# Optimization experiments

Hardware: AMD Instinct MI355X
Metric: run time of the kernel (lower is better)

Reference implementation:

```python
import jax, jax.numpy as jnp
import numpy as np

BLOCK_SIZE = 128  # config.block_size; first query block skips intra-block causal mask (faithful to source)
NEG = -1e9       # the module uses -1e9, not -inf, for masking and m_i init


def setup_inputs() -> dict:
    key = jax.random.key(0)
    kq, kk, kv, km = jax.random.split(key, 4)
    B, S, H, D = 2, 2048, 16, 64
    q = jax.random.normal(kq, (B, S, H, D), dtype=jnp.float32)
    k = jax.random.normal(kk, (B, S, H, D), dtype=jnp.float32)
    v = jax.random.normal(kv, (B, S, H, D), dtype=jnp.float32)
    mask = jax.random.randint(km, (B, S), 0, 2).astype(bool)
    mask = mask.at[:, 0].set(True)  # keep first key attendable
    return {"q": q, "k": k, "v": v, "mask": mask}


def reference(q, k, v, mask):
    # q,k,v: [B,S,H,D]; mask: [B,S] bool (True = attend)
    B, S, H, D = q.shape
    scale = 1.0 / np.sqrt(D)
    # config.normalize_query=True -> F.normalize(q, dim=-1) (eps=1e-12)
    qn = q / jnp.maximum(jnp.linalg.norm(q, axis=-1, keepdims=True), 1e-12)
    # scores: [B,S(query),H,S(key)]
    scores = jnp.einsum('bshd,bkhd->bshk', qn, k) * scale
    qi = jnp.arange(S)[:, None]
    ki = jnp.arange(S)[None, :]
    # Faithful causal structure of the blocked PyTorch fallback:
    #  - keys limited to k <= q (triu(diagonal=block_start+1) masking)
    #  - EXCEPT the first query block (block_start==0), where the intra-block
    #    causal mask is skipped (keys still limited to the first block).
    allowed = (ki <= qi) | ((qi < BLOCK_SIZE) & (ki < BLOCK_SIZE))  # [S,S]
    scores = jnp.where(allowed[None, :, None, :], scores, NEG)
    scores = jnp.where(mask[:, None, None, :], scores, NEG)
    p = jax.nn.softmax(scores, axis=-1)
    out = jnp.einsum('bshk,bkhd->bshd', p, v)
    return out
```

## Files before the change

### kernel.cpp

```cpp
#include <hip/hip_runtime.h>
#include <stdint.h>

typedef __attribute__((ext_vector_type(8))) short short8;
typedef __attribute__((ext_vector_type(4))) float floatx4;
typedef __attribute__((ext_vector_type(4))) unsigned int uintx4;
typedef __attribute__((ext_vector_type(2))) unsigned int uintx2;

#define S_LEN 2048
#define NHEAD 16
#define DHEAD 64
#define KB    64
#define NTILE 32
#define PL_BYTES (S_LEN * DHEAD * 2)
#define VOFF  (2 * NHEAD * PL_BYTES)
#define MOFF  (2 * VOFF)
#define WS_NEEDED ((size_t)MOFF + 2 * 4096)
#define NEGINF (-__builtin_inff())
#define LOG2E 1.4426950408889634f

#define GLOAD_LDS16(gp, lp) \
    __builtin_amdgcn_global_load_lds((const __attribute__((address_space(1))) unsigned int*)(gp), \
                                     (__attribute__((address_space(3))) unsigned int*)(lp), 16, 0, 0)

static __device__ __forceinline__ unsigned f2bf(float f) {
    union { float f; unsigned u; } w; w.f = f;
    return (w.u + 0x7FFFu + ((w.u >> 16) & 1u)) >> 16;
}

static __device__ __forceinline__ unsigned cvtpk(float lo, float hi) {
    unsigned r;
    asm("v_cvt_pk_bf16_f32 %0, %1, %2" : "=v"(r) : "v"(lo), "v"(hi));
    return r;
}

static __device__ __forceinline__ floatx4 mfma16(short8 a, short8 b, floatx4 c) {
    return __builtin_amdgcn_mfma_f32_16x16x32_bf16(a, b, c, 0, 0, 0);
}

__global__ __launch_bounds__(256) void prep_kernel(
    const float* __restrict__ kg, const float* __restrict__ vg,
    const int* __restrict__ mg, char* __restrict__ ws)
{
    __shared__ unsigned short Tl[64 * 72];
    const int bid = blockIdx.x;
    const int t   = bid & 31;
    const int bh  = bid >> 5;
    const int b   = bh >> 4, h = bh & 15;
    const int tid = threadIdx.x;
    char* kpre = ws + (size_t)bh * PL_BYTES;
    char* vpre = ws + VOFF + (size_t)bh * PL_BYTES;

    {
        const int r  = tid >> 2;
        const int c0 = (tid & 3) * 32;
        const int X  = (r & 7) << 4;
        const size_t grow = (((size_t)b * S_LEN + t * 64 + r) * NHEAD + h) * DHEAD;
        #pragma unroll
        for (int cc = 0; cc < 2; ++cc) {
            const int c  = c0 + 16 * cc;
            const int d0 = (c ^ X) >> 1;
            floatx4 f0 = *(const floatx4*)(kg + grow + d0);
            floatx4 f1 = *(const floatx4*)(kg + grow + d0 + 4);
            uintx4 pk = (uintx4){ f2bf(f0[0]) | (f2bf(f0[1]) << 16),
                                  f2bf(f0[2]) | (f2bf(f0[3]) << 16),
                                  f2bf(f1[0]) | (f2bf(f1[1]) << 16),
                                  f2bf(f1[2]) | (f2bf(f1[3]) << 16) };
            *(uintx4*)(kpre + t * 8192 + r * 128 + c) = pk;
        }
    }
    {
        const int key = tid >> 2;
        const int d0  = (tid & 3) * 16;
        const float vz = mg[(size_t)b * S_LEN + t * 64 + key] ? 1.f : 0.f;
        const size_t grow = (((size_t)b * S_LEN + t * 64 + key) * NHEAD + h) * DHEAD;
        #pragma unroll
        for (int q = 0; q < 4; ++q) {
            floatx4 f = *(const floatx4*)(vg + grow + d0 + 4 * q);
            #pragma unroll
            for (int ii = 0; ii < 4; ++ii)
                Tl[(d0 + 4 * q + ii) * 72 + key] = (unsigned short)f2bf(f[ii] * vz);
        }
    }
    __syncthreads();
    {
        const int d  = tid >> 2;
        const int c0 = (tid & 3) * 32;
        const int Xv = (d & 7) << 4;
        #pragma unroll
        for (int cc = 0; cc < 2; ++cc) {
            const int c   = c0 + 16 * cc;
            const int pp0 = (c ^ Xv) >> 1;
            const int blk = pp0 >> 5;
            const int a   = (pp0 & 31) >> 3;
            unsigned short vals[8];
            #pragma unroll
            for (int i = 0; i < 8; ++i) {
                const int key = 32 * blk + ((i < 4) ? (4 * a + i) : (16 + 4 * a + i - 4));
                vals[i] = Tl[d * 72 + key];
            }
            *(uintx4*)(vpre + t * 8192 + d * 128 + c) = *(const uintx4*)vals;
        }
    }
    if (h == 0 && tid < 64) {
        const int key = tid;
        const int gg = (key >> 2) & 3, lo = key & 3;
        const int ks = key >> 5,      hi = (key >> 4) & 1;
        const unsigned short mv = mg[(size_t)b * S_LEN + t * 64 + key] ? 0x3F80 : 0;
        *(unsigned short*)(ws + MOFF + (size_t)b * 4096 + t * 128
                           + gg * 32 + ks * 16 + (4 * hi + lo) * 2) = mv;
    }
}

__global__ __launch_bounds__(512, 4) void fa3_main(
    const float* __restrict__ qg, const char* __restrict__ ws,
    float* __restrict__ og)
{
    __shared__ char smem[49152];
    unsigned short* Qs = (unsigned short*)smem;
    char* KsB = smem + 16384;
    char* VsB = smem + 32768;

    const int tid  = threadIdx.x;
    const int bid  = blockIdx.x;
    const int b    = bid >> 8;
    const int bh   = (b << 4) | (bid & 15);
    const int rpair= (bid >> 4) & 15;
    const int qb   = b ? rpair : 15 - rpair;
    const int h    = bh & 15;
    const int w    = tid >> 6;
    const int lane = tid & 63;
    const int g    = lane >> 4;
    const int lm   = lane & 15;
    const int kh   = w >> 2;
    const int wq   = w & 3;
    const char* kpre = ws + (size_t)bh * PL_BYTES;
    const char* vpre = ws + VOFF + (size_t)bh * PL_BYTES;
    const char* mgf  = ws + MOFF + (size_t)b * 4096;
    const int nkt = (qb == 0) ? 2 : (2 * qb + 2);

    GLOAD_LDS16(kpre + tid * 16, KsB + tid * 16);
    GLOAD_LDS16(vpre + tid * 16, VsB + tid * 16);

    {
        const int r  = tid >> 2;
        const int q0 = tid & 3;
        const float* src = qg + (((size_t)b * S_LEN + (size_t)qb * 128 + r) * NHEAD + h) * DHEAD + q0 * 16;
        floatx4 f0 = *(const floatx4*)(src + 0);
        floatx4 f1 = *(const floatx4*)(src + 4);
        floatx4 f2 = *(const floatx4*)(src + 8);
        floatx4 f3 = *(const floatx4*)(src + 12);
        float ssq = 0.f;
        #pragma unroll
        for (int i = 0; i < 4; ++i)
            ssq += f0[i]*f0[i] + f1[i]*f1[i] + f2[i]*f2[i] + f3[i]*f3[i];
        ssq += __shfl_xor(ssq, 1);
        ssq += __shfl_xor(ssq, 2);
        const float sc = (0.125f * LOG2E) / fmaxf(sqrtf(ssq), 1e-12f);
        float fv[16];
        #pragma unroll
        for (int i = 0; i < 4; ++i) { fv[i]=f0[i]; fv[4+i]=f1[i]; fv[8+i]=f2[i]; fv[12+i]=f3[i]; }
        unsigned pk[8];
        #pragma unroll
        for (int i = 0; i < 8; ++i)
            pk[i] = cvtpk(fv[2*i]*sc, fv[2*i+1]*sc);
        const int X = (r & 7) << 4;
        char* qp = (char*)Qs + r * 128;
        *(uintx4*)(qp + ((32*q0)      ^ X)) = (uintx4){pk[0],pk[1],pk[2],pk[3]};
        *(uintx4*)(qp + ((32*q0 + 16) ^ X)) = (uintx4){pk[4],pk[5],pk[6],pk[7]};
    }
    asm volatile("s_waitcnt vmcnt(0)" ::: "memory");
    __syncthreads();

    const int Xl = (lm & 7) << 4;
    short8 qf[2][2];
    #pragma unroll
    for (int grp = 0; grp < 2; ++grp) {
        const int row = wq * 32 + grp * 16 + lm;
        const char* base = (const char*)Qs + row * 128;
        #pragma unroll
        for (int ksd = 0; ksd < 2; ++ksd)
            qf[grp][ksd] = *(const short8*)(base + ((64*ksd + 16*g) ^ Xl));
    }

    floatx4 oacc[2][4];
    floatx4 dacc[2];
    #pragma unroll
    for (int grp = 0; grp < 2; ++grp) {
        dacc[grp] = (floatx4){0.f,0.f,0.f,0.f};
        #pragma unroll
        for (int nt = 0; nt < 4; ++nt) oacc[grp][nt] = (floatx4){0.f,0.f,0.f,0.f};
    }
    const int qgl0 = qb * 128 + wq * 32 + lm;

    int cur = 0;
    for (int kt = 0; kt < nkt; ++kt) {
        if (kt + 1 < nkt) {
            const size_t tb = (size_t)(kt + 1) * 8192;
            GLOAD_LDS16(kpre + tb + tid * 16, KsB + (cur ^ 1) * 8192 + tid * 16);
            GLOAD_LDS16(vpre + tb + tid * 16, VsB + (cur ^ 1) * 8192 + tid * 16);
        }
        const short8 mf = *(const short8*)(mgf + kt * 128 + g * 32 + kh * 16);

        floatx4 st[2][2];
        #pragma unroll
        for (int grp = 0; grp < 2; ++grp)
            #pragma unroll
            for (int mt = 0; mt < 2; ++mt) st[grp][mt] = (floatx4){-8.f,-8.f,-8.f,-8.f};
        const char* kbase = KsB + cur * 8192 + kh * 4096 + lm * 128;
        __builtin_amdgcn_s_setprio(1);
        #pragma unroll
        for (int ksd = 0; ksd < 2; ++ksd) {
            #pragma unroll
            for (int mt = 0; mt < 2; ++mt) {
                short8 kf = *(const short8*)(kbase + mt * 2048 + ((64*ksd + 16*g) ^ Xl));
                st[0][mt] = mfma16(kf, qf[0][ksd], st[0][mt]);
                st[1][mt] = mfma16(kf, qf[1][ksd], st[1][mt]);
            }
        }
        __builtin_amdgcn_s_setprio(0);

        if ((qb >= 1) && (kt >= 2 * qb)) {
            #pragma unroll
            for (int mt = 0; mt < 2; ++mt)
                #pragma unroll
                for (int j = 0; j < 4; ++j) {
                    const int kgl = kt * KB + kh * 32 + mt * 16 + 4 * g + j;
                    if (kgl > qgl0)      st[0][mt][j] = -10000.f;
                    if (kgl > qgl0 + 16) st[1][mt][j] = -10000.f;
                }
        }

        short8 pa[2];
        #pragma unroll
        for (int grp = 0; grp < 2; ++grp) {
            float p[8];
            #pragma unroll
            for (int mt = 0; mt < 2; ++mt)
                #pragma unroll
                for (int j = 0; j < 4; ++j)
                    p[mt * 4 + j] = exp2f(st[grp][mt][j]);
            union { short8 s; uintx4 u; } pu;
            pu.u = (uintx4){ cvtpk(p[0], p[1]), cvtpk(p[2], p[3]),
                             cvtpk(p[4], p[5]), cvtpk(p[6], p[7]) };
            pa[grp] = pu.s;
        }
        __builtin_amdgcn_s_setprio(1);
        dacc[0] = mfma16(pa[0], mf, dacc[0]);
        dacc[1] = mfma16(pa[1], mf, dacc[1]);
        {
            const char* vbase = VsB + cur * 8192 + lm * 128;
            #pragma unroll
            for (int nt = 0; nt < 4; ++nt) {
                short8 vf = *(const short8*)(vbase + nt * 2048 + ((64*kh + 16*g) ^ Xl));
                oacc[0][nt] = mfma16(pa[0], vf, oacc[0][nt]);
                oacc[1][nt] = mfma16(pa[1], vf, oacc[1][nt]);
            }
        }
        __builtin_amdgcn_s_setprio(0);

        asm volatile("s_waitcnt vmcnt(0)" ::: "memory");
        __syncthreads();
        cur ^= 1;
    }

    floatx4* rbuf = (floatx4*)(smem + 16384);
    float*   dbuf = (float*)smem;
    if (kh == 1) {
        const int tpos = (w - 4) * 64 + lane;
        #pragma unroll
        for (int grp = 0; grp < 2; ++grp) {
            #pragma unroll
            for (int nt = 0; nt < 4; ++nt)
                rbuf[(grp * 4 + nt) * 256 + tpos] = oacc[grp][nt];
            if (lm == 0) {
                #pragma unroll
                for (int j = 0; j < 4; ++j)
                    dbuf[wq * 32 + grp * 16 + 4 * g + j] = dacc[grp][j];
            }
        }
    }
    __syncthreads();
    if (kh == 0) {
        const int tpos = w * 64 + lane;
        #pragma unroll
        for (int grp = 0; grp < 2; ++grp) {
            #pragma unroll
            for (int nt = 0; nt < 4; ++nt)
                oacc[grp][nt] += rbuf[(grp * 4 + nt) * 256 + tpos];
            #pragma unroll
            for (int j = 0; j < 4; ++j) {
                const float den = dacc[grp][j] + dbuf[wq * 32 + grp * 16 + 4 * g + j];
                const float invj = 1.0f / den;
                const int row = qb * 128 + wq * 32 + grp * 16 + 4 * g + j;
                float* dst = og + (((size_t)b * S_LEN + row) * NHEAD + h) * DHEAD + lm;
                #pragma unroll
                for (int nt = 0; nt < 4; ++nt) dst[nt * 16] = oacc[grp][nt][j] * invj;
            }
        }
    }
}

__global__ __launch_bounds__(512) void fa3_fallback(
    const float* __restrict__ qg, const float* __restrict__ kg,
    const float* __restrict__ vg, const int* __restrict__ mg,
    float* __restrict__ og)
{
    __shared__ unsigned short Qs[128 * DHEAD];
    __shared__ unsigned short Ks2[KB * DHEAD];
    __shared__ unsigned short Vt[DHEAD * KB];
    __shared__ float Ms[KB];

    const int tid  = threadIdx.x;
    const int bid  = blockIdx.x;
    const int qb   = 15 - (bid >> 5);
    const int bh   = bid & 31;
    const int b    = bh >> 4;
    const int h    = bh & 15;
    const int w    = tid >> 6;
    const int lane = tid & 63;
    const int g    = lane >> 4;
    const int lm   = lane & 15;

    {
        const int r  = tid >> 2;
        const int q0 = tid & 3;
        const float* src = qg + (((size_t)b * S_LEN + (size_t)qb * 128 + r) * NHEAD + h) * DHEAD + q0 * 16;
        floatx4 f0 = *(const floatx4*)(src + 0);
        floatx4 f1 = *(const floatx4*)(src + 4);
        floatx4 f2 = *(const floatx4*)(src + 8);
        floatx4 f3 = *(const floatx4*)(src + 12);
        float ssq = 0.f;
        #pragma unroll
        for (int i = 0; i < 4; ++i)
            ssq += f0[i]*f0[i] + f1[i]*f1[i] + f2[i]*f2[i] + f3[i]*f3[i];
        ssq += __shfl_xor(ssq, 1);
        ssq += __shfl_xor(ssq, 2);
        const float sc = 0.125f / fmaxf(sqrtf(ssq), 1e-12f);
        float fv[16];
        #pragma unroll
        for (int i = 0; i < 4; ++i) { fv[i]=f0[i]; fv[4+i]=f1[i]; fv[8+i]=f2[i]; fv[12+i]=f3[i]; }
        unsigned pk[8];
        #pragma unroll
        for (int i = 0; i < 8; ++i)
            pk[i] = f2bf(fv[2*i]*sc) | (f2bf(fv[2*i+1]*sc) << 16);
        const int X = (r & 7) << 4;
        char* qp = (char*)Qs + r * 128;
        *(uintx4*)(qp + ((32*q0)      ^ X)) = (uintx4){pk[0],pk[1],pk[2],pk[3]};
        *(uintx4*)(qp + ((32*q0 + 16) ^ X)) = (uintx4){pk[4],pk[5],pk[6],pk[7]};
    }
    __syncthreads();

    short8 qf[2];
    {
        const int row = w * 16 + lm;
        const int X = (row & 7) << 4;
        const char* base = (const char*)Qs + row * 128;
        #pragma unroll
        for (int ks = 0; ks < 2; ++ks) {
            union { short8 s; uintx2 u[2]; } u;
            u.u[0] = *(const uintx2*)(base + ((64*ks + 8*g)      ^ X));
            u.u[1] = *(const uintx2*)(base + ((64*ks + 8*g + 32) ^ X));
            qf[ks] = u.s;
        }
    }

    floatx4 oacc[4];
    #pragma unroll
    for (int nt = 0; nt < 4; ++nt) oacc[nt] = (floatx4){0.f,0.f,0.f,0.f};
    float mrun = NEGINF, lrun = 0.f;
    const int q_glob = qb * 128 + w * 16 + lm;
    const int nkt = (qb == 0) ? 2 : (2 * qb + 2);

    for (int kt = 0; kt < nkt; ++kt) {
        const int kb0 = kt * KB;
        {
            const int r = tid >> 3;
            const int o = tid & 7;
            const size_t goff = (((size_t)b * S_LEN + kb0 + r) * NHEAD + h) * DHEAD + o * 8;
            floatx4 a0 = *(const floatx4*)(kg + goff);
            floatx4 a1 = *(const floatx4*)(kg + goff + 4);
            floatx4 c0 = *(const floatx4*)(vg + goff);
            floatx4 c1 = *(const floatx4*)(vg + goff + 4);
            uintx4 kw = (uintx4){ f2bf(a0[0]) | (f2bf(a0[1])<<16),
                                  f2bf(a0[2]) | (f2bf(a0[3])<<16),
                                  f2bf(a1[0]) | (f2bf(a1[1])<<16),
                                  f2bf(a1[2]) | (f2bf(a1[3])<<16) };
            *(uintx4*)((char*)Ks2 + r*128 + ((16*o) ^ ((r & 7) << 4))) = kw;
            float cv[8];
            #pragma unroll
            for (int i = 0; i < 4; ++i) { cv[i] = c0[i]; cv[4+i] = c1[i]; }
            #pragma unroll
            for (int i = 0; i < 8; ++i) {
                const int d = 8*o + i;
                Vt[d*64 + (r ^ (((i ^ o) & 7) << 3))] = (unsigned short)f2bf(cv[i]);
            }
            if (tid < KB) Ms[tid] = mg[(size_t)b * S_LEN + kb0 + tid] ? 0.f : NEGINF;
        }
        __syncthreads();

        floatx4 st[4];
        #pragma unroll
        for (int mt = 0; mt < 4; ++mt) st[mt] = (floatx4){0.f,0.f,0.f,0.f};
        #pragma unroll
        for (int ks = 0; ks < 2; ++ks) {
            #pragma unroll
            for (int mt = 0; mt < 4; ++mt) {
                const int row = mt * 16 + lm;
                const int X = (row & 7) << 4;
                const char* base = (const char*)Ks2 + row * 128;
                union { short8 s; uintx2 u[2]; } u;
                u.u[0] = *(const uintx2*)(base + ((64*ks + 8*g)      ^ X));
                u.u[1] = *(const uintx2*)(base + ((64*ks + 8*g + 32) ^ X));
                st[mt] = mfma16(u.s, qf[ks], st[mt]);
            }
        }

        const bool diag = (qb > 0) && (kt >= 2 * qb);
        float sv[16];
        #pragma unroll
        for (int mt = 0; mt < 4; ++mt) {
            #pragma unroll
            for (int j = 0; j < 4; ++j) {
                const int kl = mt * 16 + 4 * g + j;
                float s = st[mt][j] + Ms[kl];
                if (diag && (kb0 + kl > q_glob)) s = NEGINF;
                sv[mt * 4 + j] = s;
            }
        }

        float rmax = sv[0];
        #pragma unroll
        for (int i = 1; i < 16; ++i) rmax = fmaxf(rmax, sv[i]);
        rmax = fmaxf(rmax, __shfl_xor(rmax, 16));
        rmax = fmaxf(rmax, __shfl_xor(rmax, 32));
        const float mnew = fmaxf(mrun, rmax);
        const float cf = __expf(mrun - mnew);
        float p[16], psum = 0.f;
        #pragma unroll
        for (int i = 0; i < 16; ++i) { p[i] = __expf(sv[i] - mnew); psum += p[i]; }
        psum += __shfl_xor(psum, 16);
        psum += __shfl_xor(psum, 32);
        lrun = lrun * cf + psum;
        mrun = mnew;

        float cj[4];
        #pragma unroll
        for (int j = 0; j < 4; ++j) cj[j] = __shfl(cf, 20 * g + j);
        #pragma unroll
        for (int nt = 0; nt < 4; ++nt)
            #pragma unroll
            for (int j = 0; j < 4; ++j) oacc[nt][j] *= cj[j];

        short8 pa[2];
        #pragma unroll
        for (int ks = 0; ks < 2; ++ks)
            #pragma unroll
            for (int i = 0; i < 8; ++i)
                pa[ks][i] = (short)f2bf(p[(2*ks + (i>>2))*4 + (i&3)]);

        #pragma unroll
        for (int nt = 0; nt < 4; ++nt) {
            const int d = 16 * nt + lm;
            const int xz = (((d & 7) ^ ((d >> 3) & 7)) & 7) << 4;
            const char* vb = (const char*)Vt + d * 128;
            #pragma unroll
            for (int ks = 0; ks < 2; ++ks) {
                union { short8 s; uintx2 u[2]; } vu;
                vu.u[0] = *(const uintx2*)(vb + ((64*ks + 8*g)      ^ xz));
                vu.u[1] = *(const uintx2*)(vb + ((64*ks + 8*g + 32) ^ xz));
                oacc[nt] = mfma16(pa[ks], vu.s, oacc[nt]);
            }
        }
        __syncthreads();
    }

    const float inv = 1.0f / lrun;
    #pragma unroll
    for (int j = 0; j < 4; ++j) {
        const float invj = __shfl(inv, 20 * g + j);
        const int row = qb * 128 + w * 16 + 4 * g + j;
        float* dst = og + (((size_t)b * S_LEN + row) * NHEAD + h) * DHEAD + lm;
        #pragma unroll
        for (int nt = 0; nt < 4; ++nt) dst[nt * 16] = oacc[nt][j] * invj;
    }
}

extern "C" void kernel_launch(void* const* d_in, const int* in_sizes, int n_in,
                              void* d_out, int out_size, void* d_ws, size_t ws_size,
                              hipStream_t stream)
{
    const float* q = (const float*)d_in[0];
    const float* k = (const float*)d_in[1];
    const float* v = (const float*)d_in[2];
    const int*   m = (const int*)d_in[3];
    float* out = (float*)d_out;
    (void)in_sizes; (void)n_in; (void)out_size;
    if (ws_size >= WS_NEEDED) {
        prep_kernel<<<dim3(1024), dim3(256), 0, stream>>>(k, v, m, (char*)d_ws);
        fa3_main<<<dim3(512), dim3(512), 0, stream>>>(q, (const char*)d_ws, out);
    } else {
        fa3_fallback<<<dim3(512), dim3(512), 0, stream>>>(q, k, v, m, out);
    }
}
```

Measured before the change: 50.46 us.

## Split KV range across two blocks with 256-row query tiles and combine kernel

The query tile per block grows from 128 to 256 rows, so each wave now holds four 16-row groups and every K/V fragment is reused across more MFMAs. The key range for each query tile is split into two halves handled by separate blocks. Each block writes unnormalized partial outputs and denominators to workspace, and a new combine kernel sums the two halves and normalizes. This balances causal work across blocks and raises data reuse, at the cost of an extra kernel launch, about 32MB of partial-result traffic, and higher register and LDS use (64KB LDS).

```diff
diff --git a/kernel.cpp b/kernel.cpp
--- a/kernel.cpp
+++ b/kernel.cpp
@@ -14,7 +14,11 @@
 #define PL_BYTES (S_LEN * DHEAD * 2)
 #define VOFF  (2 * NHEAD * PL_BYTES)
 #define MOFF  (2 * VOFF)
-#define WS_NEEDED ((size_t)MOFF + 2 * 4096)
+#define PO0   (MOFF + 8192)
+#define PO1   (PO0 + 256 * 65536)
+#define DN0   (PO1 + 256 * 65536)
+#define DN1   (DN0 + 262144)
+#define WS_NEEDED ((size_t)DN1 + 262144)
 #define NEGINF (-__builtin_inff())
 #define LOG2E 1.4426950408889634f
 
@@ -112,20 +116,20 @@
 }
 
 __global__ __launch_bounds__(512, 4) void fa3_main(
-    const float* __restrict__ qg, const char* __restrict__ ws,
-    float* __restrict__ og)
+    const float* __restrict__ qg, char* __restrict__ ws)
 {
-    __shared__ char smem[49152];
+    __shared__ char smem[65536];
     unsigned short* Qs = (unsigned short*)smem;
-    char* KsB = smem + 16384;
-    char* VsB = smem + 32768;
+    char* KsB = smem + 32768;
+    char* VsB = smem + 49152;
 
     const int tid  = threadIdx.x;
     const int bid  = blockIdx.x;
-    const int b    = bid >> 8;
-    const int bh   = (b << 4) | (bid & 15);
-    const int rpair= (bid >> 4) & 15;
-    const int qb   = b ? rpair : 15 - rpair;
+    const int half = bid >> 8;
+    const int r256 = bid & 255;
+    const int qb   = half ? (7 - (r256 >> 5)) : (r256 >> 5);
+    const int bh   = r256 & 31;
+    const int b    = bh >> 4;
     const int h    = bh & 15;
     const int w    = tid >> 6;
     const int lane = tid & 63;
@@ -136,15 +140,18 @@
     const char* kpre = ws + (size_t)bh * PL_BYTES;
     const char* vpre = ws + VOFF + (size_t)bh * PL_BYTES;
     const char* mgf  = ws + MOFF + (size_t)b * 4096;
-    const int nkt = (qb == 0) ? 2 : (2 * qb + 2);
-
-    GLOAD_LDS16(kpre + tid * 16, KsB + tid * 16);
-    GLOAD_LDS16(vpre + tid * 16, VsB + tid * 16);
-
-    {
-        const int r  = tid >> 2;
+    const int H   = 2 * qb + 2;
+    const int kt0 = half * H, kt1 = kt0 + H;
+    const int slot = qb * 32 + bh;
+
+    GLOAD_LDS16(kpre + (size_t)kt0 * 8192 + tid * 16, KsB + tid * 16);
+    GLOAD_LDS16(vpre + (size_t)kt0 * 8192 + tid * 16, VsB + tid * 16);
+
+    #pragma unroll
+    for (int rr = 0; rr < 2; ++rr) {
+        const int r  = rr * 128 + (tid >> 2);
         const int q0 = tid & 3;
-        const float* src = qg + (((size_t)b * S_LEN + (size_t)qb * 128 + r) * NHEAD + h) * DHEAD + q0 * 16;
+        const float* src = qg + (((size_t)b * S_LEN + (size_t)qb * 256 + r) * NHEAD + h) * DHEAD + q0 * 16;
         floatx4 f0 = *(const floatx4*)(src + 0);
         floatx4 f1 = *(const floatx4*)(src + 4);
         floatx4 f2 = *(const floatx4*)(src + 8);
@@ -172,38 +179,38 @@
     __syncthreads();
 
     const int Xl = (lm & 7) << 4;
-    short8 qf[2][2];
+    short8 qf[4][2];
     #pragma unroll
-    for (int grp = 0; grp < 2; ++grp) {
-        const int row = wq * 32 + grp * 16 + lm;
+    for (int grp = 0; grp < 4; ++grp) {
+        const int row = wq * 64 + grp * 16 + lm;
         const char* base = (const char*)Qs + row * 128;
         #pragma unroll
         for (int ksd = 0; ksd < 2; ++ksd)
             qf[grp][ksd] = *(const short8*)(base + ((64*ksd + 16*g) ^ Xl));
     }
 
-    floatx4 oacc[2][4];
-    floatx4 dacc[2];
+    floatx4 oacc[4][4];
+    floatx4 dacc[4];
     #pragma unroll
-    for (int grp = 0; grp < 2; ++grp) {
+    for (int grp = 0; grp < 4; ++grp) {
         dacc[grp] = (floatx4){0.f,0.f,0.f,0.f};
         #pragma unroll
         for (int nt = 0; nt < 4; ++nt) oacc[grp][nt] = (floatx4){0.f,0.f,0.f,0.f};
     }
-    const int qgl0 = qb * 128 + wq * 32 + lm;
+    const int qwmin = qb * 256 + wq * 64;
 
     int cur = 0;
-    for (int kt = 0; kt < nkt; ++kt) {
-        if (kt + 1 < nkt) {
+    for (int kt = kt0; kt < kt1; ++kt) {
+        if (kt + 1 < kt1) {
             const size_t tb = (size_t)(kt + 1) * 8192;
             GLOAD_LDS16(kpre + tb + tid * 16, KsB + (cur ^ 1) * 8192 + tid * 16);
             GLOAD_LDS16(vpre + tb + tid * 16, VsB + (cur ^ 1) * 8192 + tid * 16);
         }
         const short8 mf = *(const short8*)(mgf + kt * 128 + g * 32 + kh * 16);
 
-        floatx4 st[2][2];
-        #pragma unroll
-        for (int grp = 0; grp < 2; ++grp)
+        floatx4 st[4][2];
+        #pragma unroll
+        for (int grp = 0; grp < 4; ++grp)
             #pragma unroll
             for (int mt = 0; mt < 2; ++mt) st[grp][mt] = (floatx4){-8.f,-8.f,-8.f,-8.f};
         const char* kbase = KsB + cur * 8192 + kh * 4096 + lm * 128;
@@ -213,26 +220,38 @@
             #pragma unroll
             for (int mt = 0; mt < 2; ++mt) {
                 short8 kf = *(const short8*)(kbase + mt * 2048 + ((64*ksd + 16*g) ^ Xl));
-                st[0][mt] = mfma16(kf, qf[0][ksd], st[0][mt]);
-                st[1][mt] = mfma16(kf, qf[1][ksd], st[1][mt]);
+                #pragma unroll
+                for (int grp = 0; grp < 4; ++grp)
+                    st[grp][mt] = mfma16(kf, qf[grp][ksd], st[grp][mt]);
             }
         }
         __builtin_amdgcn_s_setprio(0);
 
-        if ((qb >= 1) && (kt >= 2 * qb)) {
-            #pragma unroll
-            for (int mt = 0; mt < 2; ++mt)
+        short8 vf[4];
+        {
+            const char* vbase = VsB + cur * 8192 + lm * 128;
+            #pragma unroll
+            for (int nt = 0; nt < 4; ++nt)
+                vf[nt] = *(const short8*)(vbase + nt * 2048 + ((64*kh + 16*g) ^ Xl));
+        }
+
+        if ((kt * 64 + 63 > qwmin) && (qb > 0 || kt >= 2)) {
+            #pragma unroll
+            for (int grp = 0; grp < 4; ++grp) {
+                const int qgl = qwmin + grp * 16 + lm;
                 #pragma unroll
-                for (int j = 0; j < 4; ++j) {
-                    const int kgl = kt * KB + kh * 32 + mt * 16 + 4 * g + j;
-                    if (kgl > qgl0)      st[0][mt][j] = -10000.f;
-                    if (kgl > qgl0 + 16) st[1][mt][j] = -10000.f;
-                }
-        }
-
-        short8 pa[2];
-        #pragma unroll
-        for (int grp = 0; grp < 2; ++grp) {
+                for (int mt = 0; mt < 2; ++mt)
+                    #pragma unroll
+                    for (int j = 0; j < 4; ++j) {
+                        const int kgl = kt * 64 + kh * 32 + mt * 16 + 4 * g + j;
+                        if (kgl > qgl) st[grp][mt][j] = -10000.f;
+                    }
+            }
+        }
+
+        short8 pa[4];
+        #pragma unroll
+        for (int grp = 0; grp < 4; ++grp) {
             float p[8];
             #pragma unroll
             for (int mt = 0; mt < 2; ++mt)
@@ -245,16 +264,12 @@
             pa[grp] = pu.s;
         }
         __builtin_amdgcn_s_setprio(1);
-        dacc[0] = mfma16(pa[0], mf, dacc[0]);
-        dacc[1] = mfma16(pa[1], mf, dacc[1]);
-        {
-            const char* vbase = VsB + cur * 8192 + lm * 128;
-            #pragma unroll
-            for (int nt = 0; nt < 4; ++nt) {
-                short8 vf = *(const short8*)(vbase + nt * 2048 + ((64*kh + 16*g) ^ Xl));
-                oacc[0][nt] = mfma16(pa[0], vf, oacc[0][nt]);
-                oacc[1][nt] = mfma16(pa[1], vf, oacc[1][nt]);
-            }
+        #pragma unroll
+        for (int grp = 0; grp < 4; ++grp) {
+            dacc[grp] = mfma16(pa[grp], mf, dacc[grp]);
+            #pragma unroll
+            for (int nt = 0; nt < 4; ++nt)
+                oacc[grp][nt] = mfma16(pa[grp], vf[nt], oacc[grp][nt]);
         }
         __builtin_amdgcn_s_setprio(0);
 
@@ -263,41 +278,73 @@
         cur ^= 1;
     }
 
-    floatx4* rbuf = (floatx4*)(smem + 16384);
-    float*   dbuf = (float*)smem;
+    floatx4* rbuf = (floatx4*)smem;
     if (kh == 1) {
-        const int tpos = (w - 4) * 64 + lane;
-        #pragma unroll
-        for (int grp = 0; grp < 2; ++grp) {
+        #pragma unroll
+        for (int grp = 0; grp < 4; ++grp)
             #pragma unroll
             for (int nt = 0; nt < 4; ++nt)
-                rbuf[(grp * 4 + nt) * 256 + tpos] = oacc[grp][nt];
-            if (lm == 0) {
-                #pragma unroll
-                for (int j = 0; j < 4; ++j)
-                    dbuf[wq * 32 + grp * 16 + 4 * g + j] = dacc[grp][j];
-            }
-        }
+                rbuf[wq * 1024 + (grp * 4 + nt) * 64 + lane] = oacc[grp][nt];
     }
     __syncthreads();
     if (kh == 0) {
-        const int tpos = w * 64 + lane;
-        #pragma unroll
-        for (int grp = 0; grp < 2; ++grp) {
+        #pragma unroll
+        for (int grp = 0; grp < 4; ++grp)
             #pragma unroll
             for (int nt = 0; nt < 4; ++nt)
-                oacc[grp][nt] += rbuf[(grp * 4 + nt) * 256 + tpos];
+                oacc[grp][nt] += rbuf[wq * 1024 + (grp * 4 + nt) * 64 + lane];
+    }
+    __syncthreads();
+    float* dbuf = (float*)smem;
+    if (kh == 1 && lm == 0) {
+        #pragma unroll
+        for (int grp = 0; grp < 4; ++grp)
+            #pragma unroll
+            for (int j = 0; j < 4; ++j)
+                dbuf[wq * 64 + grp * 16 + 4 * g + j] = dacc[grp][j];
+    }
+    __syncthreads();
+    if (kh == 0) {
+        float* po = (float*)(ws + (half ? PO1 : PO0) + (size_t)slot * 65536);
+        float* pd = (float*)(ws + (half ? DN1 : DN0) + (size_t)slot * 1024);
+        #pragma unroll
+        for (int grp = 0; grp < 4; ++grp)
             #pragma unroll
             for (int j = 0; j < 4; ++j) {
-                const float den = dacc[grp][j] + dbuf[wq * 32 + grp * 16 + 4 * g + j];
-                const float invj = 1.0f / den;
-                const int row = qb * 128 + wq * 32 + grp * 16 + 4 * g + j;
-                float* dst = og + (((size_t)b * S_LEN + row) * NHEAD + h) * DHEAD + lm;
+                const int row = wq * 64 + grp * 16 + 4 * g + j;
                 #pragma unroll
-                for (int nt = 0; nt < 4; ++nt) dst[nt * 16] = oacc[grp][nt][j] * invj;
-            }
-        }
-    }
+                for (int nt = 0; nt < 4; ++nt)
+                    po[row * 64 + nt * 16 + lm] = oacc[grp][nt][j];
+                if (lm == 0)
+                    pd[row] = dacc[grp][j] + dbuf[row];
+            }
+    }
+}
+
+__global__ __launch_bounds__(256) void fa3_combine(
+    const char* __restrict__ ws, float* __restrict__ og)
+{
+    const int i0  = (blockIdx.x * 256 + threadIdx.x) * 8;
+    const int d   = i0 & 63;
+    int rem       = i0 >> 6;
+    const int h   = rem & 15;  rem >>= 4;
+    const int row = rem & 2047;
+    const int b   = rem >> 11;
+    const int qb  = row >> 8;
+    const int q   = row & 255;
+    const int slot = qb * 32 + b * 16 + h;
+    const float* p0 = (const float*)(ws + PO0 + (size_t)slot * 65536) + q * 64 + d;
+    const float* p1 = (const float*)(ws + PO1 + (size_t)slot * 65536) + q * 64 + d;
+    const float den = ((const float*)(ws + DN0 + (size_t)slot * 1024))[q]
+                    + ((const float*)(ws + DN1 + (size_t)slot * 1024))[q];
+    const float inv = 1.0f / den;
+    floatx4 a0 = *(const floatx4*)p0, a1 = *(const floatx4*)(p0 + 4);
+    floatx4 b0 = *(const floatx4*)p1, b1 = *(const floatx4*)(p1 + 4);
+    floatx4 o0, o1;
+    #pragma unroll
+    for (int i = 0; i < 4; ++i) { o0[i] = (a0[i] + b0[i]) * inv; o1[i] = (a1[i] + b1[i]) * inv; }
+    *(floatx4*)(og + i0)     = o0;
+    *(floatx4*)(og + i0 + 4) = o1;
 }
 
 __global__ __launch_bounds__(512) void fa3_fallback(
@@ -497,7 +544,8 @@
     (void)in_sizes; (void)n_in; (void)out_size;
     if (ws_size >= WS_NEEDED) {
         prep_kernel<<<dim3(1024), dim3(256), 0, stream>>>(k, v, m, (char*)d_ws);
-        fa3_main<<<dim3(512), dim3(512), 0, stream>>>(q, (const char*)d_ws, out);
+        fa3_main<<<dim3(512), dim3(512), 0, stream>>>(q, (char*)d_ws);
+        fa3_combine<<<dim3(2048), dim3(256), 0, stream>>>((const char*)d_ws, out);
     } else {
         fa3_fallback<<<dim3(512), dim3(512), 0, stream>>>(q, k, v, m, out);
     }
```

New measurement: 164.5 us. 226% more time.

## Triple-buffer K/V tiles with prefetch distance two and partial vmcnt waits

Applied to the files above, without the earlier changes.

Moves the K/V LDS staging from double to triple buffering. Tiles are prefetched two iterations ahead, and each iteration waits with a partial vmcnt before a single barrier instead of draining all loads and syncing at the end of the loop. The mask fragment is also loaded one tile ahead, and the first QK MFMA takes a constant -8 accumulator directly. The epilogue reduction gets a different rbuf indexing and extra barriers. This cuts load-latency stalls per iteration, at the cost of LDS rising from 48KB to 64KB, which may lower occupancy below the 4 blocks the launch bounds request.

```diff
diff --git a/kernel.cpp b/kernel.cpp
--- a/kernel.cpp
+++ b/kernel.cpp
@@ -115,10 +115,10 @@
     const float* __restrict__ qg, const char* __restrict__ ws,
     float* __restrict__ og)
 {
-    __shared__ char smem[49152];
+    __shared__ char smem[65536];
     unsigned short* Qs = (unsigned short*)smem;
     char* KsB = smem + 16384;
-    char* VsB = smem + 32768;
+    char* VsB = smem + 40960;
 
     const int tid  = threadIdx.x;
     const int bid  = blockIdx.x;
@@ -168,7 +168,6 @@
         *(uintx4*)(qp + ((32*q0)      ^ X)) = (uintx4){pk[0],pk[1],pk[2],pk[3]};
         *(uintx4*)(qp + ((32*q0 + 16) ^ X)) = (uintx4){pk[4],pk[5],pk[6],pk[7]};
     }
-    asm volatile("s_waitcnt vmcnt(0)" ::: "memory");
     __syncthreads();
 
     const int Xl = (lm & 7) << 4;
@@ -182,6 +181,12 @@
             qf[grp][ksd] = *(const short8*)(base + ((64*ksd + 16*g) ^ Xl));
     }
 
+    short8 mfn = *(const short8*)(mgf + 0 * 128 + g * 32 + kh * 16);
+    if (nkt > 1) {
+        GLOAD_LDS16(kpre + 8192 + tid * 16, KsB + 8192 + tid * 16);
+        GLOAD_LDS16(vpre + 8192 + tid * 16, VsB + 8192 + tid * 16);
+    }
+
     floatx4 oacc[2][4];
     floatx4 dacc[2];
     #pragma unroll
@@ -190,32 +195,41 @@
         #pragma unroll
         for (int nt = 0; nt < 4; ++nt) oacc[grp][nt] = (floatx4){0.f,0.f,0.f,0.f};
     }
+    floatx4 NEG8 = (floatx4){-8.f,-8.f,-8.f,-8.f};
+    asm volatile("" : "+v"(NEG8));
     const int qgl0 = qb * 128 + wq * 32 + lm;
 
     int cur = 0;
     for (int kt = 0; kt < nkt; ++kt) {
-        if (kt + 1 < nkt) {
-            const size_t tb = (size_t)(kt + 1) * 8192;
-            GLOAD_LDS16(kpre + tb + tid * 16, KsB + (cur ^ 1) * 8192 + tid * 16);
-            GLOAD_LDS16(vpre + tb + tid * 16, VsB + (cur ^ 1) * 8192 + tid * 16);
-        }
-        const short8 mf = *(const short8*)(mgf + kt * 128 + g * 32 + kh * 16);
+        if (kt + 1 < nkt) { asm volatile("s_waitcnt vmcnt(2)" ::: "memory"); }
+        else              { asm volatile("s_waitcnt vmcnt(0)" ::: "memory"); }
+        __builtin_amdgcn_s_barrier();
+        __builtin_amdgcn_sched_barrier(0);
+
+        const short8 mf = mfn;
+        if (kt + 1 < nkt)
+            mfn = *(const short8*)(mgf + (kt + 1) * 128 + g * 32 + kh * 16);
+        if (kt + 2 < nkt) {
+            int nb = cur + 2; if (nb >= 3) nb -= 3;
+            const size_t tb = (size_t)(kt + 2) * 8192;
+            GLOAD_LDS16(kpre + tb + tid * 16, KsB + nb * 8192 + tid * 16);
+            GLOAD_LDS16(vpre + tb + tid * 16, VsB + nb * 8192 + tid * 16);
+        }
 
         floatx4 st[2][2];
-        #pragma unroll
-        for (int grp = 0; grp < 2; ++grp)
-            #pragma unroll
-            for (int mt = 0; mt < 2; ++mt) st[grp][mt] = (floatx4){-8.f,-8.f,-8.f,-8.f};
         const char* kbase = KsB + cur * 8192 + kh * 4096 + lm * 128;
         __builtin_amdgcn_s_setprio(1);
         #pragma unroll
-        for (int ksd = 0; ksd < 2; ++ksd) {
-            #pragma unroll
-            for (int mt = 0; mt < 2; ++mt) {
-                short8 kf = *(const short8*)(kbase + mt * 2048 + ((64*ksd + 16*g) ^ Xl));
-                st[0][mt] = mfma16(kf, qf[0][ksd], st[0][mt]);
-                st[1][mt] = mfma16(kf, qf[1][ksd], st[1][mt]);
-            }
+        for (int mt = 0; mt < 2; ++mt) {
+            short8 kf = *(const short8*)(kbase + mt * 2048 + ((16*g) ^ Xl));
+            st[0][mt] = mfma16(kf, qf[0][0], NEG8);
+            st[1][mt] = mfma16(kf, qf[1][0], NEG8);
+        }
+        #pragma unroll
+        for (int mt = 0; mt < 2; ++mt) {
+            short8 kf = *(const short8*)(kbase + mt * 2048 + ((64 + 16*g) ^ Xl));
+            st[0][mt] = mfma16(kf, qf[0][1], st[0][mt]);
+            st[1][mt] = mfma16(kf, qf[1][1], st[1][mt]);
         }
         __builtin_amdgcn_s_setprio(0);
 
@@ -258,35 +272,39 @@
         }
         __builtin_amdgcn_s_setprio(0);
 
-        asm volatile("s_waitcnt vmcnt(0)" ::: "memory");
-        __syncthreads();
-        cur ^= 1;
-    }
+        cur += 1; if (cur >= 3) cur -= 3;
+    }
+    __syncthreads();
 
     floatx4* rbuf = (floatx4*)(smem + 16384);
     float*   dbuf = (float*)smem;
     if (kh == 1) {
-        const int tpos = (w - 4) * 64 + lane;
-        #pragma unroll
-        for (int grp = 0; grp < 2; ++grp) {
+        #pragma unroll
+        for (int grp = 0; grp < 2; ++grp)
             #pragma unroll
             for (int nt = 0; nt < 4; ++nt)
-                rbuf[(grp * 4 + nt) * 256 + tpos] = oacc[grp][nt];
-            if (lm == 0) {
-                #pragma unroll
-                for (int j = 0; j < 4; ++j)
-                    dbuf[wq * 32 + grp * 16 + 4 * g + j] = dacc[grp][j];
-            }
-        }
+                rbuf[((grp * 4 + nt) * 4 + wq) * 64 + lane] = oacc[grp][nt];
     }
     __syncthreads();
     if (kh == 0) {
-        const int tpos = w * 64 + lane;
-        #pragma unroll
-        for (int grp = 0; grp < 2; ++grp) {
+        #pragma unroll
+        for (int grp = 0; grp < 2; ++grp)
             #pragma unroll
             for (int nt = 0; nt < 4; ++nt)
-                oacc[grp][nt] += rbuf[(grp * 4 + nt) * 256 + tpos];
+                oacc[grp][nt] += rbuf[((grp * 4 + nt) * 4 + wq) * 64 + lane];
+    }
+    __syncthreads();
+    if (kh == 1 && lm == 0) {
+        #pragma unroll
+        for (int grp = 0; grp < 2; ++grp)
+            #pragma unroll
+            for (int j = 0; j < 4; ++j)
+                dbuf[wq * 32 + grp * 16 + 4 * g + j] = dacc[grp][j];
+    }
+    __syncthreads();
+    if (kh == 0) {
+        #pragma unroll
+        for (int grp = 0; grp < 2; ++grp)
             #pragma unroll
             for (int j = 0; j < 4; ++j) {
                 const float den = dacc[grp][j] + dbuf[wq * 32 + grp * 16 + 4 * g + j];
@@ -296,7 +314,6 @@
                 #pragma unroll
                 for (int nt = 0; nt < 4; ++nt) dst[nt * 16] = oacc[grp][nt][j] * invj;
             }
-        }
     }
 }
 
```

Result: no change. 51.28 us (+1.6%).
